# Kernel tuning notes

Measured on AMD Instinct MI355X. Metric: run time of the kernel, lower is better.

The kernel has to match this reference:

```python
import jax, jax.numpy as jnp
import numpy as np

B, T, IN, OUT = 8, 2048, 1024, 512
DT, TAU = 1.0, 20.0


def setup_inputs() -> dict:
    key = jax.random.key(0)
    k1, k2 = jax.random.split(key)
    x = jax.random.normal(k1, (B, T, IN), jnp.float32)
    lim = 1.0 / np.sqrt(IN)
    weight = jax.random.uniform(k2, (OUT, IN), jnp.float32, -lim, lim)
    bias = jnp.zeros((OUT,), jnp.float32)
    # fixed tau trainer: decay = exp(-dt / tau) per output feature
    decay = jnp.full((OUT,), float(np.exp(-DT / TAU)), jnp.float32)
    return {"input_tensor": x, "weight": weight, "bias": bias, "decay": decay}


def reference(input_tensor, weight, bias, decay):
    # Hoist the time-invariant GEMM out of the recurrence: [B,T,OUT]
    current = jnp.einsum('bti,oi->bto', input_tensor, weight) + bias
    v0 = jnp.zeros((input_tensor.shape[0], weight.shape[0]), input_tensor.dtype)

    def step(v_tm1, c_t):
        v_t = decay * v_tm1 + (1.0 - decay) * c_t
        return v_t, v_t

    # scan over time axis: [T,B,OUT]
    _, outs = jax.lax.scan(step, v0, jnp.swapaxes(current, 0, 1))
    outputs = jnp.swapaxes(outs, 0, 1)  # [B,T,OUT]
    states = jnp.concatenate([v0[:, None, :], outputs], axis=1)[None]  # [1,B,T+1,OUT]
    return outputs, states
```

## Files before the change

kernel.cpp:

```cpp
#include <hip/hip_runtime.h>
#include <hip/hip_bf16.h>
#include <cstddef>
#include <cstdint>

#define BB    8
#define TT    2048
#define KIN   1024
#define NOUT  512
#define CHUNK 32
#define NCHUNK (TT / CHUNK)

#define BM 128
#define BN 128
#define BK 32
#define NKSTEP (KIN / BK)
#define TILEB 8192

typedef __attribute__((ext_vector_type(4))) float          f32x4;
typedef __attribute__((ext_vector_type(4))) unsigned int   u32x4;
typedef _Float16 f16x8 __attribute__((ext_vector_type(8)));

__global__ __launch_bounds__(256) void conv_tiled_f16(
    const float* __restrict__ src, unsigned char* __restrict__ dst, int total) {
  int idx = blockIdx.x * blockDim.x + threadIdx.x;
  const int stride = gridDim.x * blockDim.x;
  for (; idx < total; idx += stride) {
    const int r  = idx >> 7;
    const int s8 = idx & 127;
    const float* p = src + (size_t)r * KIN + s8 * 8;
    float4 a = *reinterpret_cast<const float4*>(p);
    float4 b = *reinterpret_cast<const float4*>(p + 4);
    f16x8 h;
    h[0] = (_Float16)a.x; h[1] = (_Float16)a.y;
    h[2] = (_Float16)a.z; h[3] = (_Float16)a.w;
    h[4] = (_Float16)b.x; h[5] = (_Float16)b.y;
    h[6] = (_Float16)b.z; h[7] = (_Float16)b.w;
    const int row  = r & 127;
    const int tile = (r >> 7) * NKSTEP + (s8 >> 2);
    const int slot = (s8 & 3) ^ ((row >> 1) & 3);
    *reinterpret_cast<f16x8*>(dst + (size_t)tile * TILEB + row * 64 + slot * 16) = h;
  }
}

#define G2L(gp, sp)                                                        \
  __builtin_amdgcn_global_load_lds(                                       \
      (const __attribute__((address_space(1))) void*)(gp),                \
      (__attribute__((address_space(3))) void*)(sp), 16, 0, 0)

__global__ __launch_bounds__(256, 2) void gemm_f16(
    const unsigned char* __restrict__ Xt, const unsigned char* __restrict__ Wt,
    const float* __restrict__ bias, const float* __restrict__ decay,
    float* __restrict__ C, float* __restrict__ vend) {
  __shared__ __align__(16) unsigned char smem[2 * TILEB];

  const int tid  = threadIdx.x;
  const int wave = tid >> 6;
  const int lane = tid & 63;
  const int m0 = blockIdx.x * BM;
  const int n0 = blockIdx.y * BN;
  const int wm = (wave >> 1) * 64;
  const int wn = (wave & 1) * 64;
  const int frow = lane & 15;
  const int g    = lane >> 4;

  unsigned char* sA = smem;
  unsigned char* sB = smem + TILEB;

  const unsigned char* srcA = Xt + (size_t)(m0 >> 7) * NKSTEP * TILEB + tid * 16;
  const unsigned char* srcB = Wt + (size_t)(n0 >> 7) * NKSTEP * TILEB + tid * 16;
  const int ldsw = wave * 1024;

  const int swzr = (g ^ ((frow >> 1) & 3)) << 4;

  f32x4 acc[4][4] = {};

  for (int t = 0; t < NKSTEP; ++t) {
    __syncthreads();
    const size_t toff = (size_t)t * TILEB;
    G2L(srcA + toff,        sA + ldsw);
    G2L(srcA + toff + 4096, sA + 4096 + ldsw);
    G2L(srcB + toff,        sB + ldsw);
    G2L(srcB + toff + 4096, sB + 4096 + ldsw);
    __syncthreads();

    f16x8 af[4];
#pragma unroll
    for (int mi = 0; mi < 4; ++mi)
      af[mi] = *reinterpret_cast<const f16x8*>(sA + (wm + mi * 16 + frow) * 64 + swzr);
#pragma unroll
    for (int ni = 0; ni < 4; ++ni) {
      f16x8 bf = *reinterpret_cast<const f16x8*>(sB + (wn + ni * 16 + frow) * 64 + swzr);
#pragma unroll
      for (int mi = 0; mi < 4; ++mi)
        acc[mi][ni] = __builtin_amdgcn_mfma_f32_16x16x32_f16(af[mi], bf, acc[mi][ni], 0, 0, 0);
    }
  }

  const int colb = n0 + wn + frow;
  const int rowb = m0 + wm + (g << 2);
  float bv[4];
#pragma unroll
  for (int ni = 0; ni < 4; ++ni) bv[ni] = bias[colb + ni * 16];
#pragma unroll
  for (int mi = 0; mi < 4; ++mi) {
#pragma unroll
    for (int r = 0; r < 4; ++r) {
#pragma unroll
      for (int ni = 0; ni < 4; ++ni)
        C[(size_t)(rowb + mi * 16 + r) * NOUT + colb + ni * 16] = acc[mi][ni][r] + bv[ni];
    }
  }

  {
    float rlo[4], rhi[4];
#pragma unroll
    for (int ni = 0; ni < 4; ++ni) {
      const float d  = decay[colb + ni * 16];
      const float bb = bv[ni];
      const float omd = 1.0f - d;
      const float dd = d * d, d4 = dd * dd, d8 = d4 * d4;
      const float d16 = d8 * d8, d12 = d8 * d4;
      const float dpg = (g == 0) ? d12 : (g == 1) ? d8 : (g == 2) ? d4 : 1.0f;
      float s[4];
#pragma unroll
      for (int mi = 0; mi < 4; ++mi) {
        float v = acc[mi][ni][0] + bb;
        v = v * d + (acc[mi][ni][1] + bb);
        v = v * d + (acc[mi][ni][2] + bb);
        v = v * d + (acc[mi][ni][3] + bb);
        s[mi] = omd * v;
      }
      float ulo = dpg * (s[0] * d16 + s[1]);
      float uhi = dpg * (s[2] * d16 + s[3]);
      ulo += __shfl_xor(ulo, 16); ulo += __shfl_xor(ulo, 32);
      uhi += __shfl_xor(uhi, 16); uhi += __shfl_xor(uhi, 32);
      rlo[ni] = ulo; rhi[ni] = uhi;
    }
    const int b   = m0 >> 11;
    const int clo = ((m0 & (TT - 1)) >> 5) + (wm >> 5);
    const int chunk = clo + (g >> 1);
    const int half  = g >> 1;
    const int nia   = g & 1;
    const float v1 = half ? (nia ? rhi[1] : rhi[0]) : (nia ? rlo[1] : rlo[0]);
    const float v2 = half ? (nia ? rhi[3] : rhi[2]) : (nia ? rlo[3] : rlo[2]);
    const int col1 = n0 + wn + frow + nia * 16;
    float* vp = vend + ((size_t)b * NCHUNK + chunk) * NOUT;
    vp[col1]      = v1;
    vp[col1 + 32] = v2;
  }
}

__global__ __launch_bounds__(256) void gemm_f32_64x64(
    const float* __restrict__ X, const float* __restrict__ W,
    const float* __restrict__ bias, float* __restrict__ C) {
  __shared__ float As[16][65];
  __shared__ float Bs[16][65];
  const int m0  = blockIdx.y * 64;
  const int n0  = blockIdx.x * 64;
  const int tid = threadIdx.x;
  const int tx  = tid & 15;
  const int ty  = tid >> 4;
  const int lr  = tid >> 2;
  const int lk  = (tid & 3) << 2;
  float acc[4][4] = {};
  const float* xa = X + (size_t)(m0 + lr) * KIN + lk;
  const float* wb = W + (size_t)(n0 + lr) * KIN + lk;
  for (int k0 = 0; k0 < KIN; k0 += 16) {
    float4 av = *reinterpret_cast<const float4*>(xa + k0);
    float4 bv = *reinterpret_cast<const float4*>(wb + k0);
    As[lk + 0][lr] = av.x; As[lk + 1][lr] = av.y;
    As[lk + 2][lr] = av.z; As[lk + 3][lr] = av.w;
    Bs[lk + 0][lr] = bv.x; Bs[lk + 1][lr] = bv.y;
    Bs[lk + 2][lr] = bv.z; Bs[lk + 3][lr] = bv.w;
    __syncthreads();
#pragma unroll
    for (int k = 0; k < 16; ++k) {
      float a[4], b[4];
#pragma unroll
      for (int i = 0; i < 4; ++i) a[i] = As[k][ty * 4 + i];
#pragma unroll
      for (int j = 0; j < 4; ++j) b[j] = Bs[k][tx * 4 + j];
#pragma unroll
      for (int i = 0; i < 4; ++i)
#pragma unroll
        for (int j = 0; j < 4; ++j) acc[i][j] += a[i] * b[j];
    }
    __syncthreads();
  }
  const int n = n0 + tx * 4;
  float4 bv = *reinterpret_cast<const float4*>(&bias[n]);
#pragma unroll
  for (int i = 0; i < 4; ++i) {
    const int m = m0 + ty * 4 + i;
    float4 r;
    r.x = acc[i][0] + bv.x; r.y = acc[i][1] + bv.y;
    r.z = acc[i][2] + bv.z; r.w = acc[i][3] + bv.w;
    *reinterpret_cast<float4*>(&C[(size_t)m * NOUT + n]) = r;
  }
}

__global__ __launch_bounds__(512) void scan_chunks(
    const float* __restrict__ vend, const float* __restrict__ decay,
    float* __restrict__ vinit) {
  const int b = blockIdx.x;
  const int o = threadIdx.x;
  const float d = decay[o];
  float d2 = d * d, d4 = d2 * d2, d8 = d4 * d4, d16 = d8 * d8;
  const float dL = d16 * d16;
  float V = 0.0f;
  for (int c = 0; c < NCHUNK; ++c) {
    const size_t idx = ((size_t)b * NCHUNK + c) * NOUT + o;
    vinit[idx] = V;
    V = dL * V + vend[idx];
  }
}

__global__ __launch_bounds__(512) void scan_fixup(
    float* __restrict__ C, float* __restrict__ states,
    const float* __restrict__ decay, const float* __restrict__ vinit) {
  const int b = blockIdx.x / NCHUNK;
  const int c = blockIdx.x % NCHUNK;
  const int o = threadIdx.x;
  const float d   = decay[o];
  const float omd = 1.0f - d;
  float v = vinit[((size_t)b * NCHUNK + c) * NOUT + o];
  size_t obase = ((size_t)b * TT + (size_t)c * CHUNK) * NOUT + o;
  size_t sbase = ((size_t)b * (TT + 1) + (size_t)c * CHUNK + 1) * NOUT + o;
#pragma unroll 4
  for (int k = 0; k < CHUNK; ++k) {
    v = d * v + omd * C[obase + (size_t)k * NOUT];
    C[obase + (size_t)k * NOUT]      = v;
    states[sbase + (size_t)k * NOUT] = v;
  }
  if (c == 0) states[((size_t)b * (TT + 1)) * NOUT + o] = 0.0f;
}

__global__ __launch_bounds__(512) void scan_seq(
    float* __restrict__ C, float* __restrict__ states,
    const float* __restrict__ decay) {
  const int b = blockIdx.x;
  const int o = threadIdx.x;
  const float d   = decay[o];
  const float omd = 1.0f - d;
  float v = 0.0f;
  states[((size_t)b * (TT + 1)) * NOUT + o] = 0.0f;
  for (int t = 0; t < TT; ++t) {
    const size_t oi = ((size_t)b * TT + t) * NOUT + o;
    float x = C[oi];
    v = d * v + omd * x;
    C[oi] = v;
    states[((size_t)b * (TT + 1) + t + 1) * NOUT + o] = v;
  }
}

extern "C" void kernel_launch(void* const* d_in, const int* in_sizes, int n_in,
                              void* d_out, int out_size, void* d_ws, size_t ws_size,
                              hipStream_t stream) {
  const float* x     = (const float*)d_in[0];
  const float* w     = (const float*)d_in[1];
  const float* bias  = (const float*)d_in[2];
  const float* decay = (const float*)d_in[3];

  float* out    = (float*)d_out;
  float* states = out + (size_t)BB * TT * NOUT;

  const size_t szXb = (size_t)BB * TT * KIN * sizeof(_Float16);
  const size_t szWb = (size_t)NOUT * KIN * sizeof(_Float16);
  const size_t scan_elems = (size_t)BB * NCHUNK * NOUT;
  const size_t need = szXb + szWb + 2 * scan_elems * sizeof(float);

  if (ws_size >= need) {
    unsigned char* Xt = (unsigned char*)d_ws;
    unsigned char* Wt = Xt + szXb;
    float* vend  = (float*)(Wt + szWb);
    float* vinit = vend + scan_elems;

    conv_tiled_f16<<<2048, 256, 0, stream>>>(x, Xt, BB * TT * (KIN / 8));
    conv_tiled_f16<<<256,  256, 0, stream>>>(w, Wt, NOUT * (KIN / 8));
    gemm_f16<<<dim3((BB * TT) / BM, NOUT / BN), 256, 0, stream>>>(
        Xt, Wt, bias, decay, out, vend);
    scan_chunks<<<BB, NOUT, 0, stream>>>(vend, decay, vinit);
    scan_fixup <<<BB * NCHUNK, NOUT, 0, stream>>>(out, states, decay, vinit);
  } else {
    gemm_f32_64x64<<<dim3(NOUT / 64, (BB * TT) / 64), 256, 0, stream>>>(x, w, bias, out);
    scan_seq<<<BB, NOUT, 0, stream>>>(out, states, decay);
  }
}
```

Baseline: 71.17 us.

## Store GEMM output as fp16, fuse chunk scan into fixup, double K-step

The GEMM now stages two 32-wide K pages per barrier (BK=64), which halves the number of sync points. It writes the pre-scan current as fp16 into a workspace instead of fp32 into the output. The separate chunk-prefix kernel is removed: each fixup block recomputes its starting state by serially folding the preceding chunk ends, which saves one launch and the vinit round trip. The fp16 intermediate adds rounding error to the recurrence input, and later chunks do more redundant serial prefix work.

Result: faster. 69.60 us (-2.2%).

```diff
diff --git a/kernel.cpp b/kernel.cpp
--- a/kernel.cpp
+++ b/kernel.cpp
@@ -12,8 +12,9 @@
 
 #define BM 128
 #define BN 128
-#define BK 32
+#define BK 64
 #define NKSTEP (KIN / BK)
+#define NPAGE  (KIN / 32)
 #define TILEB 8192
 
 typedef __attribute__((ext_vector_type(4))) float          f32x4;
@@ -36,9 +37,9 @@
     h[4] = (_Float16)b.x; h[5] = (_Float16)b.y;
     h[6] = (_Float16)b.z; h[7] = (_Float16)b.w;
     const int row  = r & 127;
-    const int tile = (r >> 7) * NKSTEP + (s8 >> 2);
+    const int page = (r >> 7) * NPAGE + (s8 >> 2);
     const int slot = (s8 & 3) ^ ((row >> 1) & 3);
-    *reinterpret_cast<f16x8*>(dst + (size_t)tile * TILEB + row * 64 + slot * 16) = h;
+    *reinterpret_cast<f16x8*>(dst + (size_t)page * TILEB + row * 64 + slot * 16) = h;
   }
 }
 
@@ -50,8 +51,8 @@
 __global__ __launch_bounds__(256, 2) void gemm_f16(
     const unsigned char* __restrict__ Xt, const unsigned char* __restrict__ Wt,
     const float* __restrict__ bias, const float* __restrict__ decay,
-    float* __restrict__ C, float* __restrict__ vend) {
-  __shared__ __align__(16) unsigned char smem[2 * TILEB];
+    unsigned short* __restrict__ Cws, float* __restrict__ vend) {
+  __shared__ __align__(16) unsigned char smem[2 * 16384];
 
   const int tid  = threadIdx.x;
   const int wave = tid >> 6;
@@ -64,10 +65,10 @@
   const int g    = lane >> 4;
 
   unsigned char* sA = smem;
-  unsigned char* sB = smem + TILEB;
-
-  const unsigned char* srcA = Xt + (size_t)(m0 >> 7) * NKSTEP * TILEB + tid * 16;
-  const unsigned char* srcB = Wt + (size_t)(n0 >> 7) * NKSTEP * TILEB + tid * 16;
+  unsigned char* sB = smem + 16384;
+
+  const unsigned char* srcA = Xt + (size_t)(m0 >> 7) * NPAGE * TILEB + tid * 16;
+  const unsigned char* srcB = Wt + (size_t)(n0 >> 7) * NPAGE * TILEB + tid * 16;
   const int ldsw = wave * 1024;
 
   const int swzr = (g ^ ((frow >> 1) & 3)) << 4;
@@ -76,23 +77,29 @@
 
   for (int t = 0; t < NKSTEP; ++t) {
     __syncthreads();
-    const size_t toff = (size_t)t * TILEB;
-    G2L(srcA + toff,        sA + ldsw);
-    G2L(srcA + toff + 4096, sA + 4096 + ldsw);
-    G2L(srcB + toff,        sB + ldsw);
-    G2L(srcB + toff + 4096, sB + 4096 + ldsw);
-    __syncthreads();
-
-    f16x8 af[4];
-#pragma unroll
-    for (int mi = 0; mi < 4; ++mi)
-      af[mi] = *reinterpret_cast<const f16x8*>(sA + (wm + mi * 16 + frow) * 64 + swzr);
-#pragma unroll
-    for (int ni = 0; ni < 4; ++ni) {
-      f16x8 bf = *reinterpret_cast<const f16x8*>(sB + (wn + ni * 16 + frow) * 64 + swzr);
+    const size_t toff = (size_t)(2 * t) * TILEB;
+#pragma unroll
+    for (int q = 0; q < 4; ++q) {
+      G2L(srcA + toff + q * 4096, sA + q * 4096 + ldsw);
+      G2L(srcB + toff + q * 4096, sB + q * 4096 + ldsw);
+    }
+    __syncthreads();
+
+#pragma unroll
+    for (int kk = 0; kk < 2; ++kk) {
+      f16x8 af[4];
 #pragma unroll
       for (int mi = 0; mi < 4; ++mi)
-        acc[mi][ni] = __builtin_amdgcn_mfma_f32_16x16x32_f16(af[mi], bf, acc[mi][ni], 0, 0, 0);
+        af[mi] = *reinterpret_cast<const f16x8*>(
+            sA + kk * 8192 + (wm + mi * 16 + frow) * 64 + swzr);
+#pragma unroll
+      for (int ni = 0; ni < 4; ++ni) {
+        f16x8 bf = *reinterpret_cast<const f16x8*>(
+            sB + kk * 8192 + (wn + ni * 16 + frow) * 64 + swzr);
+#pragma unroll
+        for (int mi = 0; mi < 4; ++mi)
+          acc[mi][ni] = __builtin_amdgcn_mfma_f32_16x16x32_f16(af[mi], bf, acc[mi][ni], 0, 0, 0);
+      }
     }
   }
 
@@ -106,8 +113,11 @@
 #pragma unroll
     for (int r = 0; r < 4; ++r) {
 #pragma unroll
-      for (int ni = 0; ni < 4; ++ni)
-        C[(size_t)(rowb + mi * 16 + r) * NOUT + colb + ni * 16] = acc[mi][ni][r] + bv[ni];
+      for (int ni = 0; ni < 4; ++ni) {
+        const _Float16 hv = (_Float16)(acc[mi][ni][r] + bv[ni]);
+        Cws[(size_t)(rowb + mi * 16 + r) * NOUT + colb + ni * 16] =
+            __builtin_bit_cast(unsigned short, hv);
+      }
     }
   }
 
@@ -199,37 +209,30 @@
   }
 }
 
-__global__ __launch_bounds__(512) void scan_chunks(
-    const float* __restrict__ vend, const float* __restrict__ decay,
-    float* __restrict__ vinit) {
-  const int b = blockIdx.x;
-  const int o = threadIdx.x;
-  const float d = decay[o];
-  float d2 = d * d, d4 = d2 * d2, d8 = d4 * d4, d16 = d8 * d8;
-  const float dL = d16 * d16;
-  float V = 0.0f;
-  for (int c = 0; c < NCHUNK; ++c) {
-    const size_t idx = ((size_t)b * NCHUNK + c) * NOUT + o;
-    vinit[idx] = V;
-    V = dL * V + vend[idx];
-  }
-}
-
-__global__ __launch_bounds__(512) void scan_fixup(
-    float* __restrict__ C, float* __restrict__ states,
-    const float* __restrict__ decay, const float* __restrict__ vinit) {
+__global__ __launch_bounds__(512) void scan_fixup2(
+    const unsigned short* __restrict__ Cws, const float* __restrict__ vend,
+    const float* __restrict__ decay, float* __restrict__ out,
+    float* __restrict__ states) {
   const int b = blockIdx.x / NCHUNK;
   const int c = blockIdx.x % NCHUNK;
   const int o = threadIdx.x;
   const float d   = decay[o];
   const float omd = 1.0f - d;
-  float v = vinit[((size_t)b * NCHUNK + c) * NOUT + o];
+  const float dd = d * d, d4 = dd * dd, d8 = d4 * d4, d16 = d8 * d8;
+  const float dL = d16 * d16;
+
+  float v = 0.0f;
+  const float* vp = vend + (size_t)b * NCHUNK * NOUT + o;
+  for (int cc = 0; cc < c; ++cc) v = dL * v + vp[(size_t)cc * NOUT];
+
   size_t obase = ((size_t)b * TT + (size_t)c * CHUNK) * NOUT + o;
   size_t sbase = ((size_t)b * (TT + 1) + (size_t)c * CHUNK + 1) * NOUT + o;
 #pragma unroll 4
   for (int k = 0; k < CHUNK; ++k) {
-    v = d * v + omd * C[obase + (size_t)k * NOUT];
-    C[obase + (size_t)k * NOUT]      = v;
+    const unsigned short hu = Cws[obase + (size_t)k * NOUT];
+    const float cur = (float)__builtin_bit_cast(_Float16, hu);
+    v = d * v + omd * cur;
+    out[obase + (size_t)k * NOUT]    = v;
     states[sbase + (size_t)k * NOUT] = v;
   }
   if (c == 0) states[((size_t)b * (TT + 1)) * NOUT + o] = 0.0f;
@@ -266,21 +269,21 @@
 
   const size_t szXb = (size_t)BB * TT * KIN * sizeof(_Float16);
   const size_t szWb = (size_t)NOUT * KIN * sizeof(_Float16);
+  const size_t szCb = (size_t)BB * TT * NOUT * sizeof(_Float16);
   const size_t scan_elems = (size_t)BB * NCHUNK * NOUT;
-  const size_t need = szXb + szWb + 2 * scan_elems * sizeof(float);
+  const size_t need = szXb + szWb + szCb + scan_elems * sizeof(float);
 
   if (ws_size >= need) {
-    unsigned char* Xt = (unsigned char*)d_ws;
-    unsigned char* Wt = Xt + szXb;
-    float* vend  = (float*)(Wt + szWb);
-    float* vinit = vend + scan_elems;
+    unsigned char*  Xt  = (unsigned char*)d_ws;
+    unsigned char*  Wt  = Xt + szXb;
+    unsigned short* Cws = (unsigned short*)(Wt + szWb);
+    float*          vend = (float*)(Cws + (size_t)BB * TT * NOUT);
 
     conv_tiled_f16<<<2048, 256, 0, stream>>>(x, Xt, BB * TT * (KIN / 8));
     conv_tiled_f16<<<256,  256, 0, stream>>>(w, Wt, NOUT * (KIN / 8));
     gemm_f16<<<dim3((BB * TT) / BM, NOUT / BN), 256, 0, stream>>>(
-        Xt, Wt, bias, decay, out, vend);
-    scan_chunks<<<BB, NOUT, 0, stream>>>(vend, decay, vinit);
-    scan_fixup <<<BB * NCHUNK, NOUT, 0, stream>>>(out, states, decay, vinit);
+        Xt, Wt, bias, decay, Cws, vend);
+    scan_fixup2<<<BB * NCHUNK, NOUT, 0, stream>>>(Cws, vend, decay, out, states);
   } else {
     gemm_f32_64x64<<<dim3(NOUT / 64, (BB * TT) / 64), 256, 0, stream>>>(x, w, bias, out);
     scan_seq<<<BB, NOUT, 0, stream>>>(out, states, decay);
```
